# Performance work log

Hardware: AMD Instinct MI355X
Metric: run time of the kernel (lower is better)

The kernel has to match this reference:

```python
import jax, jax.numpy as jnp
import numpy as np

N = 25000      # nodes
E = 400000     # edges
IN = 1024      # in_channels
FC = 128       # feature_channels
ADD = 20       # additional_channels
MID = (FC + ADD) // 4   # 37, fc1 output (heads=4)
OUT = 3
EPS = 1e-5
NEG_SLOPE = 0.01


def setup_inputs() -> dict:
    key = jax.random.key(0)
    ks = jax.random.split(key, 16)
    d = {}
    d["features"] = jax.random.normal(ks[0], (N, IN), dtype=jnp.float32)
    d["edges"] = jax.random.randint(ks[1], (2, E), 0, N, dtype=jnp.int64)
    d["edges2"] = jax.random.randint(ks[2], (2, 1000), 0, N, dtype=jnp.int64)
    d["edge_features"] = jax.random.normal(ks[3], (E, 1), dtype=jnp.float32)
    d["additional_feature"] = jax.random.normal(ks[4], (N, ADD), dtype=jnp.float32)
    # SAGEConv params: lin_l (neighbor path, with bias), lin_r (root path, no bias)
    s = 1.0 / np.sqrt(IN)
    d["Wl"] = jax.random.uniform(ks[5], (FC, IN), jnp.float32, -s, s)
    d["bl"] = jax.random.uniform(ks[6], (FC,), jnp.float32, -s, s)
    d["Wr"] = jax.random.uniform(ks[7], (FC, IN), jnp.float32, -s, s)
    s1 = 1.0 / np.sqrt(FC + ADD)
    d["W1"] = jax.random.uniform(ks[8], (MID, FC + ADD), jnp.float32, -s1, s1)
    d["b1"] = jax.random.uniform(ks[9], (MID,), jnp.float32, -s1, s1)
    s2 = 1.0 / np.sqrt(MID)
    d["W2"] = jax.random.uniform(ks[10], (OUT, MID), jnp.float32, -s2, s2)
    d["b2"] = jax.random.uniform(ks[11], (OUT,), jnp.float32, -s2, s2)
    # BatchNorm1d (eval mode -> running stats)
    d["gamma"] = jnp.ones((MID,), jnp.float32)
    d["beta"] = jnp.zeros((MID,), jnp.float32)
    d["run_mean"] = jax.random.normal(ks[12], (MID,), dtype=jnp.float32) * 0.1
    d["run_var"] = jnp.abs(jax.random.normal(ks[13], (MID,), dtype=jnp.float32)) * 0.1 + 1.0
    return d


def reference(features, edges, edges2, edge_features, additional_feature,
              Wl, bl, Wr, W1, b1, W2, b2, gamma, beta, run_mean, run_var):
    src, dst = edges[0], edges[1]  # PyG: messages flow source -> target
    # scatter-mean of neighbor features onto targets
    agg = jax.ops.segment_sum(features[src], dst, num_segments=N)        # [N, IN]
    deg = jax.ops.segment_sum(jnp.ones((E,), features.dtype), dst, num_segments=N)
    agg = agg / jnp.maximum(deg, 1.0)[:, None]
    # SAGEConv: lin_l(mean_neigh) + lin_r(x)
    x = agg @ Wl.T + bl + features @ Wr.T                                 # [N, FC]
    x = jnp.where(x >= 0, x, NEG_SLOPE * x)                               # leaky_relu
    # dropout is identity in eval mode
    x = jnp.concatenate([x, additional_feature], axis=1) @ W1.T + b1      # [N, MID]
    x = jnp.maximum(x, 0.0)                                               # relu
    x = gamma * (x - run_mean) * jax.lax.rsqrt(run_var + EPS) + beta      # BN eval
    return x @ W2.T + b2                                                  # [N, OUT]
```

## Files before the change

kernel.cpp:

```cpp
#include <hip/hip_runtime.h>

#define N_NODES 25000
#define N_EDGES 400000
#define IN_CH 1024
#define FC 128
#define ADD_CH 20
#define XCH 148
#define MID 37
#define OUT_CH 3
#define MAXDEG 64

typedef short bf16x8 __attribute__((ext_vector_type(8)));
typedef float f32x4 __attribute__((ext_vector_type(4)));

__device__ __forceinline__ unsigned int f2bf(float x) {
    unsigned int u = __builtin_bit_cast(unsigned int, x);
    unsigned int lsb = (u >> 16) & 1u;
    u += 0x7fffu + lsb;
    return u >> 16;
}
__device__ __forceinline__ unsigned int pkbf(float a, float b) {
    return f2bf(a) | (f2bf(b) << 16);
}
__device__ __forceinline__ float bflo(unsigned int v) {
    return __builtin_bit_cast(float, v << 16);
}
__device__ __forceinline__ float bfhi(unsigned int v) {
    return __builtin_bit_cast(float, v & 0xffff0000u);
}

__device__ __forceinline__ void gload16(const void* g, void* l) {
    __builtin_amdgcn_global_load_lds(
        (const __attribute__((address_space(1))) unsigned int*)g,
        (__attribute__((address_space(3))) unsigned int*)l,
        16, 0, 0);
}

#define WSWZ_B 16
#define BUILD_B 782

__global__ __launch_bounds__(512) void prep_build(const float* __restrict__ Wl,
                                                  const float* __restrict__ Wr,
                                                  ushort* __restrict__ Wpk,
                                                  const int* __restrict__ edges,
                                                  int* __restrict__ cursor,
                                                  int* __restrict__ col) {
    int b = blockIdx.x, t = threadIdx.x;
    if (b < WSWZ_B) {
        int w = t >> 6, lane = t & 63, l15 = lane & 15, q8 = (lane >> 4) * 8;
        int ch = b * 16 + l15;
        const float* src = (ch < FC) ? (Wl + (size_t)ch * IN_CH)
                                     : (Wr + (size_t)(ch - FC) * IN_CH);
        #pragma unroll
        for (int j = 0; j < 4; ++j) {
            int kt = w * 4 + j;
            float4 lo = *(const float4*)(src + kt * 32 + q8);
            float4 hi = *(const float4*)(src + kt * 32 + q8 + 4);
            uint4 pk;
            pk.x = pkbf(lo.x, lo.y); pk.y = pkbf(lo.z, lo.w);
            pk.z = pkbf(hi.x, hi.y); pk.w = pkbf(hi.z, hi.w);
            ((uint4*)Wpk)[((size_t)kt * 16 + b) * 64 + lane] = pk;
        }
    } else {
        int e = (b - WSWZ_B) * 512 + t;
        if (e < N_EDGES) {
            int dst = edges[N_EDGES + e];
            int pos = atomicAdd(&cursor[dst], 1);
            if (pos < MAXDEG) col[dst * MAXDEG + pos] = edges[e];
        }
    }
}

#define GEMM_B 391

__global__ __launch_bounds__(512, 6) void gemm(const float* __restrict__ A,
                                               const ushort* __restrict__ Wpk,
                                               ushort* __restrict__ Py,
                                               ushort* __restrict__ Pz) {
    __shared__ uint4 LDS[2][1536];
    int t = threadIdx.x;
    int b = blockIdx.x;
    int m0 = b * 64;

    int ga = t >> 7, hq = (t >> 6) & 1, la = t & 63;
    int nodeA = m0 + ga * 16 + (la & 15);
    if (nodeA >= N_NODES) nodeA = N_NODES - 1;
    const float* Asrc = A + (size_t)nodeA * IN_CH + (la >> 4) * 8 + hq * 4;
    const uint4* Wg = (const uint4*)Wpk;
    int tb = t & ~63;

    int w = t >> 6, lane = t & 63;
    int wm = w >> 2, wn = w & 3;
    int l15 = lane & 15, q = lane >> 4;

    f32x4 acc[4][2] = {};

    {
        const uint4* ws = Wg;
        gload16(ws + t,        &LDS[0][tb]);
        gload16(ws + 512 + t,  &LDS[0][512 + tb]);
        gload16(Asrc,          &LDS[0][1024 + tb]);
    }
    __syncthreads();

    for (int c = 0; c < 32; ++c) {
        int cur = c & 1;
        if (c + 1 < 32) {
            const uint4* ws = Wg + (size_t)(c + 1) * 1024;
            gload16(ws + t,       &LDS[cur ^ 1][tb]);
            gload16(ws + 512 + t, &LDS[cur ^ 1][512 + tb]);
            gload16(Asrc + (size_t)(c + 1) * 32, &LDS[cur ^ 1][1024 + tb]);
        }
        bf16x8 wf[4];
        #pragma unroll
        for (int i = 0; i < 4; ++i)
            wf[i] = *(const bf16x8*)&LDS[cur][(wn * 4 + i) * 64 + lane];
        bf16x8 af[2];
        #pragma unroll
        for (int g2 = 0; g2 < 2; ++g2) {
            f32x4 lo = *(const f32x4*)&LDS[cur][1024 + ((wm * 2 + g2) * 2 + 0) * 64 + lane];
            f32x4 hi = *(const f32x4*)&LDS[cur][1024 + ((wm * 2 + g2) * 2 + 1) * 64 + lane];
            uint4 pk;
            pk.x = pkbf(lo[0], lo[1]); pk.y = pkbf(lo[2], lo[3]);
            pk.z = pkbf(hi[0], hi[1]); pk.w = pkbf(hi[2], hi[3]);
            af[g2] = __builtin_bit_cast(bf16x8, pk);
        }
        #pragma unroll
        for (int i = 0; i < 4; ++i)
            #pragma unroll
            for (int g2 = 0; g2 < 2; ++g2)
                acc[i][g2] = __builtin_amdgcn_mfma_f32_16x16x32_bf16(wf[i], af[g2], acc[i][g2], 0, 0, 0);
        __syncthreads();
    }

    #pragma unroll
    for (int g2 = 0; g2 < 2; ++g2) {
        int node = m0 + wm * 32 + g2 * 16 + l15;
        if (node < N_NODES) {
            ushort* base = (wn < 2) ? (Py + (size_t)node * FC + (wn & 1) * 64 + q * 4)
                                    : (Pz + (size_t)node * FC + (wn & 1) * 64 + q * 4);
            #pragma unroll
            for (int i = 0; i < 4; ++i) {
                f32x4 v = acc[i][g2];
                uint2 pk;
                pk.x = pkbf(v[0], v[1]);
                pk.y = pkbf(v[2], v[3]);
                *(uint2*)(base + i * 16) = pk;
            }
        }
    }
}

__global__ __launch_bounds__(256) void fused_tail(const ushort* __restrict__ Py,
                                                  const ushort* __restrict__ Pz,
                                                  const int* __restrict__ deg,
                                                  const int* __restrict__ col,
                                                  const float* __restrict__ addf,
                                                  const float* __restrict__ bl,
                                                  const float* __restrict__ W1,
                                                  const float* __restrict__ b1,
                                                  const float* __restrict__ W2,
                                                  const float* __restrict__ b2,
                                                  const float* __restrict__ gamma,
                                                  const float* __restrict__ beta,
                                                  const float* __restrict__ rmean,
                                                  const float* __restrict__ rvar,
                                                  float* __restrict__ out) {
    __shared__ float W1s[XCH][MID + 3];
    __shared__ float xbuf[4][XCH + 4];
    __shared__ float hbuf[4][MID + 3];
    int t = threadIdx.x;
    for (int idx = t; idx < MID * XCH; idx += 256) {
        int j = idx / XCH, k = idx - j * XCH;
        W1s[k][j] = W1[idx];
    }
    __syncthreads();
    int w = t >> 6, lane = t & 63;
    int n = blockIdx.x * 4 + w;
    bool valid = (n < N_NODES);
    int d = valid ? deg[n] : 0;
    if (d > MAXDEG) d = MAXDEG;
    int g = lane >> 4, c16 = lane & 15;
    float s[8] = {0.f, 0.f, 0.f, 0.f, 0.f, 0.f, 0.f, 0.f};
    if (d > 0) {
        int cidx = col[n * MAXDEG + (lane < d ? lane : 0)];
        for (int i = 0; i < d; i += 16) {
            int e[4];
            uint4 v[4];
            #pragma unroll
            for (int j = 0; j < 4; ++j) {
                int ee = i + g + j * 4;
                e[j] = __shfl(cidx, (ee < d) ? ee : 0);
            }
            #pragma unroll
            for (int j = 0; j < 4; ++j)
                v[j] = *(const uint4*)&Py[(size_t)e[j] * FC + c16 * 8];
            #pragma unroll
            for (int j = 0; j < 4; ++j) {
                if (i + g + j * 4 < d) {
                    s[0] += bflo(v[j].x); s[1] += bfhi(v[j].x);
                    s[2] += bflo(v[j].y); s[3] += bfhi(v[j].y);
                    s[4] += bflo(v[j].z); s[5] += bfhi(v[j].z);
                    s[6] += bflo(v[j].w); s[7] += bfhi(v[j].w);
                }
            }
        }
        #pragma unroll
        for (int r = 0; r < 8; ++r) {
            s[r] += __shfl_xor(s[r], 16);
            s[r] += __shfl_xor(s[r], 32);
        }
    }
    if (valid) {
        if (lane < 16) {
            #pragma unroll
            for (int r = 0; r < 8; ++r) xbuf[w][lane * 8 + r] = s[r];
        }
        float invd = 1.0f / (float)(d > 1 ? d : 1);
        unsigned int vr = *(const unsigned int*)&Pz[(size_t)n * FC + lane * 2];
        float x0 = xbuf[w][2 * lane] * invd + bl[2 * lane] + bflo(vr);
        float x1 = xbuf[w][2 * lane + 1] * invd + bl[2 * lane + 1] + bfhi(vr);
        x0 = (x0 >= 0.f) ? x0 : 0.01f * x0;
        x1 = (x1 >= 0.f) ? x1 : 0.01f * x1;
        xbuf[w][2 * lane] = x0;
        xbuf[w][2 * lane + 1] = x1;
        if (lane < ADD_CH) xbuf[w][FC + lane] = addf[(size_t)n * ADD_CH + lane];
        if (lane < MID) {
            float h = b1[lane];
            #pragma unroll 4
            for (int k = 0; k < XCH; ++k) h += W1s[k][lane] * xbuf[w][k];
            h = fmaxf(h, 0.0f);
            h = gamma[lane] * (h - rmean[lane]) * rsqrtf(rvar[lane] + 1e-5f) + beta[lane];
            hbuf[w][lane] = h;
        }
        if (lane < OUT_CH) {
            float o = b2[lane];
            #pragma unroll
            for (int j = 0; j < MID; ++j) o += W2[lane * MID + j] * hbuf[w][j];
            out[(size_t)n * OUT_CH + lane] = o;
        }
    }
}


extern "C" void kernel_launch(void* const* d_in, const int* in_sizes, int n_in,
                              void* d_out, int out_size, void* d_ws, size_t ws_size,
                              hipStream_t stream) {
    const float* features = (const float*)d_in[0];
    const int*   edges    = (const int*)d_in[1];
    const float* addf     = (const float*)d_in[4];
    const float* Wl       = (const float*)d_in[5];
    const float* bl       = (const float*)d_in[6];
    const float* Wr       = (const float*)d_in[7];
    const float* W1       = (const float*)d_in[8];
    const float* b1       = (const float*)d_in[9];
    const float* W2       = (const float*)d_in[10];
    const float* b2       = (const float*)d_in[11];
    const float* gamma    = (const float*)d_in[12];
    const float* beta     = (const float*)d_in[13];
    const float* rmean    = (const float*)d_in[14];
    const float* rvar     = (const float*)d_in[15];
    float* out = (float*)d_out;

    char* ws = (char*)d_ws;
    size_t off = 0;
    ushort* Py = (ushort*)(ws + off);     off += (size_t)N_NODES * FC * 2;
    ushort* Pz = (ushort*)(ws + off);     off += (size_t)N_NODES * FC * 2;
    ushort* Wpk = (ushort*)(ws + off);    off += (size_t)32 * 16 * 64 * 16;
    int* cursor = (int*)(ws + off);       off += (size_t)N_NODES * 4;
    int* col = (int*)(ws + off);          off += (size_t)N_NODES * MAXDEG * 4;

    hipMemsetAsync(cursor, 0, (size_t)N_NODES * 4, stream);

    prep_build<<<WSWZ_B + BUILD_B, 512, 0, stream>>>(Wl, Wr, Wpk, edges, cursor, col);

    gemm<<<GEMM_B, 512, 0, stream>>>(features, Wpk, Py, Pz);

    fused_tail<<<(N_NODES + 3) / 4, 256, 0, stream>>>(Py, Pz, cursor, col, addf, bl,
                                                      W1, b1, W2, b2, gamma, beta,
                                                      rmean, rvar, out);
}
```

Measured before the change: 273.5 us.

## Fuse graph build into GEMM launch, use hardware bf16 convert, drop memset

Replaces the hipMemsetAsync with zeroing the cursor array inside the weight-swizzle prep kernel. The edge-bucketing work moves out of prep and into extra blocks of the GEMM launch, so it overlaps with the GEMM. The software round-to-nearest bf16 packing is replaced with the v_cvt_pk_bf16_f32 instruction. The GEMM occupancy hint drops from 6 to 4, and the tail kernel now uses 512-thread blocks covering 8 nodes. The aim is fewer launches, less serialized prep work and cheaper conversions, at the cost of different occupancy and possible contention between atomic-heavy blocks and GEMM blocks.

```diff
diff --git a/kernel.cpp b/kernel.cpp
--- a/kernel.cpp
+++ b/kernel.cpp
@@ -13,20 +13,16 @@
 typedef short bf16x8 __attribute__((ext_vector_type(8)));
 typedef float f32x4 __attribute__((ext_vector_type(4)));
 
-__device__ __forceinline__ unsigned int f2bf(float x) {
-    unsigned int u = __builtin_bit_cast(unsigned int, x);
-    unsigned int lsb = (u >> 16) & 1u;
-    u += 0x7fffu + lsb;
-    return u >> 16;
-}
-__device__ __forceinline__ unsigned int pkbf(float a, float b) {
-    return f2bf(a) | (f2bf(b) << 16);
-}
 __device__ __forceinline__ float bflo(unsigned int v) {
     return __builtin_bit_cast(float, v << 16);
 }
 __device__ __forceinline__ float bfhi(unsigned int v) {
     return __builtin_bit_cast(float, v & 0xffff0000u);
+}
+__device__ __forceinline__ unsigned int cvtpk(float a, float b) {
+    unsigned int r;
+    asm("v_cvt_pk_bf16_f32 %0, %1, %2" : "=v"(r) : "v"(a), "v"(b));
+    return r;
 }
 
 __device__ __forceinline__ void gload16(const void* g, void* l) {
@@ -37,14 +33,12 @@
 }
 
 #define WSWZ_B 16
-#define BUILD_B 782
-
-__global__ __launch_bounds__(512) void prep_build(const float* __restrict__ Wl,
-                                                  const float* __restrict__ Wr,
-                                                  ushort* __restrict__ Wpk,
-                                                  const int* __restrict__ edges,
-                                                  int* __restrict__ cursor,
-                                                  int* __restrict__ col) {
+#define ZERO_B 49
+
+__global__ __launch_bounds__(512) void prep(const float* __restrict__ Wl,
+                                            const float* __restrict__ Wr,
+                                            ushort* __restrict__ Wpk,
+                                            int* __restrict__ cursor) {
     int b = blockIdx.x, t = threadIdx.x;
     if (b < WSWZ_B) {
         int w = t >> 6, lane = t & 63, l15 = lane & 15, q8 = (lane >> 4) * 8;
@@ -57,29 +51,37 @@
             float4 lo = *(const float4*)(src + kt * 32 + q8);
             float4 hi = *(const float4*)(src + kt * 32 + q8 + 4);
             uint4 pk;
-            pk.x = pkbf(lo.x, lo.y); pk.y = pkbf(lo.z, lo.w);
-            pk.z = pkbf(hi.x, hi.y); pk.w = pkbf(hi.z, hi.w);
+            pk.x = cvtpk(lo.x, lo.y); pk.y = cvtpk(lo.z, lo.w);
+            pk.z = cvtpk(hi.x, hi.y); pk.w = cvtpk(hi.z, hi.w);
             ((uint4*)Wpk)[((size_t)kt * 16 + b) * 64 + lane] = pk;
         }
     } else {
-        int e = (b - WSWZ_B) * 512 + t;
+        int i = (b - WSWZ_B) * 512 + t;
+        if (i < N_NODES) cursor[i] = 0;
+    }
+}
+
+#define GEMM_B 391
+#define BUILD_B 782
+
+__global__ __launch_bounds__(512, 4) void gemm_build(const float* __restrict__ A,
+                                                     const ushort* __restrict__ Wpk,
+                                                     ushort* __restrict__ Py,
+                                                     ushort* __restrict__ Pz,
+                                                     const int* __restrict__ edges,
+                                                     int* __restrict__ cursor,
+                                                     int* __restrict__ col) {
+    __shared__ uint4 LDS[2][1536];
+    int b = blockIdx.x, t = threadIdx.x;
+    if (b >= GEMM_B) {
+        int e = (b - GEMM_B) * 512 + t;
         if (e < N_EDGES) {
             int dst = edges[N_EDGES + e];
             int pos = atomicAdd(&cursor[dst], 1);
             if (pos < MAXDEG) col[dst * MAXDEG + pos] = edges[e];
         }
-    }
-}
-
-#define GEMM_B 391
-
-__global__ __launch_bounds__(512, 6) void gemm(const float* __restrict__ A,
-                                               const ushort* __restrict__ Wpk,
-                                               ushort* __restrict__ Py,
-                                               ushort* __restrict__ Pz) {
-    __shared__ uint4 LDS[2][1536];
-    int t = threadIdx.x;
-    int b = blockIdx.x;
+        return;
+    }
     int m0 = b * 64;
 
     int ga = t >> 7, hq = (t >> 6) & 1, la = t & 63;
@@ -95,12 +97,9 @@
 
     f32x4 acc[4][2] = {};
 
-    {
-        const uint4* ws = Wg;
-        gload16(ws + t,        &LDS[0][tb]);
-        gload16(ws + 512 + t,  &LDS[0][512 + tb]);
-        gload16(Asrc,          &LDS[0][1024 + tb]);
-    }
+    gload16(Wg + t,       &LDS[0][tb]);
+    gload16(Wg + 512 + t, &LDS[0][512 + tb]);
+    gload16(Asrc,         &LDS[0][1024 + tb]);
     __syncthreads();
 
     for (int c = 0; c < 32; ++c) {
@@ -121,8 +120,8 @@
             f32x4 lo = *(const f32x4*)&LDS[cur][1024 + ((wm * 2 + g2) * 2 + 0) * 64 + lane];
             f32x4 hi = *(const f32x4*)&LDS[cur][1024 + ((wm * 2 + g2) * 2 + 1) * 64 + lane];
             uint4 pk;
-            pk.x = pkbf(lo[0], lo[1]); pk.y = pkbf(lo[2], lo[3]);
-            pk.z = pkbf(hi[0], hi[1]); pk.w = pkbf(hi[2], hi[3]);
+            pk.x = cvtpk(lo[0], lo[1]); pk.y = cvtpk(lo[2], lo[3]);
+            pk.z = cvtpk(hi[0], hi[1]); pk.w = cvtpk(hi[2], hi[3]);
             af[g2] = __builtin_bit_cast(bf16x8, pk);
         }
         #pragma unroll
@@ -143,15 +142,15 @@
             for (int i = 0; i < 4; ++i) {
                 f32x4 v = acc[i][g2];
                 uint2 pk;
-                pk.x = pkbf(v[0], v[1]);
-                pk.y = pkbf(v[2], v[3]);
+                pk.x = cvtpk(v[0], v[1]);
+                pk.y = cvtpk(v[2], v[3]);
                 *(uint2*)(base + i * 16) = pk;
             }
         }
     }
 }
 
-__global__ __launch_bounds__(256) void fused_tail(const ushort* __restrict__ Py,
+__global__ __launch_bounds__(512) void fused_tail(const ushort* __restrict__ Py,
                                                   const ushort* __restrict__ Pz,
                                                   const int* __restrict__ deg,
                                                   const int* __restrict__ col,
@@ -167,16 +166,16 @@
                                                   const float* __restrict__ rvar,
                                                   float* __restrict__ out) {
     __shared__ float W1s[XCH][MID + 3];
-    __shared__ float xbuf[4][XCH + 4];
-    __shared__ float hbuf[4][MID + 3];
+    __shared__ float xbuf[8][XCH + 4];
+    __shared__ float hbuf[8][MID + 3];
     int t = threadIdx.x;
-    for (int idx = t; idx < MID * XCH; idx += 256) {
+    for (int idx = t; idx < MID * XCH; idx += 512) {
         int j = idx / XCH, k = idx - j * XCH;
         W1s[k][j] = W1[idx];
     }
     __syncthreads();
     int w = t >> 6, lane = t & 63;
-    int n = blockIdx.x * 4 + w;
+    int n = blockIdx.x * 8 + w;
     bool valid = (n < N_NODES);
     int d = valid ? deg[n] : 0;
     if (d > MAXDEG) d = MAXDEG;
@@ -270,13 +269,12 @@
     int* cursor = (int*)(ws + off);       off += (size_t)N_NODES * 4;
     int* col = (int*)(ws + off);          off += (size_t)N_NODES * MAXDEG * 4;
 
-    hipMemsetAsync(cursor, 0, (size_t)N_NODES * 4, stream);
-
-    prep_build<<<WSWZ_B + BUILD_B, 512, 0, stream>>>(Wl, Wr, Wpk, edges, cursor, col);
-
-    gemm<<<GEMM_B, 512, 0, stream>>>(features, Wpk, Py, Pz);
-
-    fused_tail<<<(N_NODES + 3) / 4, 256, 0, stream>>>(Py, Pz, cursor, col, addf, bl,
+    prep<<<WSWZ_B + ZERO_B, 512, 0, stream>>>(Wl, Wr, Wpk, cursor);
+
+    gemm_build<<<GEMM_B + BUILD_B, 512, 0, stream>>>(features, Wpk, Py, Pz,
+                                                     edges, cursor, col);
+
+    fused_tail<<<(N_NODES + 7) / 8, 512, 0, stream>>>(Py, Pz, cursor, col, addf, bl,
                                                       W1, b1, W2, b2, gamma, beta,
                                                       rmean, rvar, out);
 }
```

Result: no change. 268.4 us (-1.8%).
